# Kernel optimization log

Hardware: AMD Instinct MI355X
Metric: run time of the kernel (lower is better)

The kernel has to match this reference:

```python
import jax, jax.numpy as jnp
import numpy as np

N_NODES = 100000
N_EDGES = 1600000
IN_DIM = 256
HEAD_DIM = 64  # out_dim // num_heads = 256 // 4
NEG_SLOPE = 0.01  # F.leaky_relu default


def setup_inputs() -> dict:
    key = jax.random.key(0)
    k1, k2, k3, k4, k5, k6 = jax.random.split(key, 6)
    h = jax.random.normal(k1, (N_NODES, IN_DIM), dtype=jnp.float32)
    snorm_n = jax.random.uniform(k2, (N_NODES, 1), dtype=jnp.float32)
    fc_w = jax.random.normal(k3, (HEAD_DIM, IN_DIM), dtype=jnp.float32) * (1.0 / np.sqrt(IN_DIM))
    attn_w = jax.random.normal(k4, (1, 2 * HEAD_DIM), dtype=jnp.float32) * (1.0 / np.sqrt(2 * HEAD_DIM))
    src = jax.random.randint(k5, (N_EDGES,), 0, N_NODES, dtype=jnp.int64 if jax.config.jax_enable_x64 else jnp.int32)
    dst = jax.random.randint(k6, (N_EDGES,), 0, N_NODES, dtype=jnp.int64 if jax.config.jax_enable_x64 else jnp.int32)
    return {"h": h, "snorm_n": snorm_n, "fc_w": fc_w, "attn_w": attn_w, "src": src, "dst": dst}


def reference(h, snorm_n, fc_w, attn_w, src, dst):
    N = h.shape[0]
    z = h @ fc_w.T  # [N, d]
    d = z.shape[1]
    # attn_fc(cat([z_src, z_dst])) == z_src @ w_l + z_dst @ w_r
    w_l, w_r = attn_w[0, :d], attn_w[0, d:]
    el = z @ w_l  # [N]
    er = z @ w_r  # [N]
    e = jax.nn.leaky_relu(el[src] + er[dst], NEG_SLOPE)  # [E] edge scores
    # segment softmax over incoming edges of each dst node
    m = jax.ops.segment_max(e, dst, num_segments=N)
    m = jnp.where(jnp.isfinite(m), m, 0.0)  # empty segments -> -inf, neutralize
    ex = jnp.exp(e - m[dst])
    denom = jax.ops.segment_sum(ex, dst, num_segments=N)
    alpha = ex / denom[dst]  # [E]
    # weighted scatter-sum of source features
    h_out = jax.ops.segment_sum(alpha[:, None] * z[src], dst, num_segments=N)  # [N, d]
    h_out = h_out * snorm_n  # graph_norm
    return jax.nn.relu(h_out)
```

## Files before the change

kernel.cpp:

```cpp
#include <hip/hip_runtime.h>
#include <math.h>

#define NEG_SLOPE 0.01f
#define NB 256
#define BATCH 4096
#define HROW 264

typedef __attribute__((ext_vector_type(8))) short short8;
typedef __attribute__((ext_vector_type(4))) float f32x4;

__device__ __forceinline__ unsigned short f2bf_rne(float f) {
    unsigned u = __float_as_uint(f);
    unsigned r = 0x7fffu + ((u >> 16) & 1u);
    return (unsigned short)((u + r) >> 16);
}
__device__ __forceinline__ float bf2f(unsigned short b) {
    return __uint_as_float(((unsigned)b) << 16);
}
__device__ __forceinline__ unsigned cvtpk(float lo, float hi) {
    unsigned r;
    asm("v_cvt_pk_bf16_f32 %0, %1, %2" : "=v"(r) : "v"(lo), "v"(hi));
    return r;
}

__global__ __launch_bounds__(256) void k_hist(
    const int* __restrict__ dst, int* __restrict__ hist_blk, int n_edges,
    const float* __restrict__ fc_w,
    unsigned short* __restrict__ w_hi, unsigned short* __restrict__ w_lo, int wdim)
{
    const int tid = threadIdx.x;
    const int nbatch = (n_edges + BATCH - 1) / BATCH;
    if ((int)blockIdx.x < nbatch) {
        __shared__ int hist[NB];
        const int batch = blockIdx.x;
        hist[tid] = 0;
        __syncthreads();
        const int e0 = batch * BATCH;
        const int n = min(BATCH, n_edges - e0);
        #pragma unroll
        for (int k = 0; k < 16; ++k) {
            int j = tid + k * 256;
            if (j < n) atomicAdd(&hist[dst[e0 + j] >> 9], 1);
        }
        __syncthreads();
        hist_blk[batch * NB + tid] = hist[tid];
    } else {
        int i = (blockIdx.x - nbatch) * 256 + tid;
        if (i < wdim) {
            float f = fc_w[i];
            unsigned u = __float_as_uint(f);
            w_hi[i] = (unsigned short)(u >> 16);
            float lo = f - __uint_as_float(u & 0xffff0000u);
            w_lo[i] = f2bf_rne(lo);
        }
    }
}

__global__ __launch_bounds__(256) void k_p2loc(
    const int* __restrict__ hist_blk, int* __restrict__ bb,
    int* __restrict__ bucket_tot, int n_edges)
{
    const int tid = threadIdx.x;
    const int b = blockIdx.x;
    const int nbatch = (n_edges + BATCH - 1) / BATCH;
    __shared__ int v[512], s2[256];
    v[tid]       = (tid < nbatch)       ? hist_blk[tid * NB + b]         : 0;
    v[tid + 256] = (tid + 256 < nbatch) ? hist_blk[(tid + 256) * NB + b] : 0;
    __syncthreads();
    int pair = v[2 * tid] + v[2 * tid + 1];
    s2[tid] = pair;
    __syncthreads();
    for (int off = 1; off < 256; off <<= 1) {
        int t = (tid >= off) ? s2[tid - off] : 0;
        __syncthreads();
        s2[tid] += t;
        __syncthreads();
    }
    int e2 = s2[tid] - pair;
    if (2 * tid < nbatch)     bb[b * nbatch + 2 * tid]     = e2;
    if (2 * tid + 1 < nbatch) bb[b * nbatch + 2 * tid + 1] = e2 + v[2 * tid];
    if (tid == 255) bucket_tot[b] = s2[255];
}

__global__ __launch_bounds__(256) void k_p2a(
    const int* __restrict__ bucket_tot, int* __restrict__ bucket_base)
{
    const int tid = threadIdx.x;
    __shared__ int a[NB];
    int tot = bucket_tot[tid];
    a[tid] = tot;
    __syncthreads();
    for (int off = 1; off < NB; off <<= 1) {
        int t = (tid >= off) ? a[tid - off] : 0;
        __syncthreads();
        a[tid] += t;
        __syncthreads();
    }
    bucket_base[tid] = a[tid] - tot;
    if (tid == NB - 1) bucket_base[NB] = a[tid];
}

__global__ __launch_bounds__(256) void k_p3convgemm(
    const int* __restrict__ src, const int* __restrict__ dst,
    const int* __restrict__ bb, const int* __restrict__ bucket_base,
    unsigned* __restrict__ rec1, int n_edges,
    const float* __restrict__ h,
    const unsigned short* __restrict__ w_hi, const unsigned short* __restrict__ w_lo,
    const float* __restrict__ attn_w,
    unsigned short* __restrict__ z_bf16, float* __restrict__ el, float* __restrict__ er,
    int n_nodes)
{
    __shared__ __align__(16) char smem[24832];
    const int tid = threadIdx.x;
    const int nbatch = (n_edges + BATCH - 1) / BATCH;

    if ((int)blockIdx.x < nbatch) {
        int* hist  = (int*)smem;
        int* offs  = hist + NB;
        int* cnt2  = offs + NB;
        int* gbase = cnt2 + NB;
        unsigned* staged = (unsigned*)(gbase + NB);
        unsigned char* sbkt = (unsigned char*)(staged + BATCH);
        const int batch = blockIdx.x;
        const int e0 = batch * BATCH;
        const int n = min(BATCH, n_edges - e0);
        hist[tid] = 0; cnt2[tid] = 0;
        gbase[tid] = bucket_base[tid] + bb[tid * nbatch + batch];
        __syncthreads();
        int d[16], s[16];
        #pragma unroll
        for (int k = 0; k < 16; ++k) {
            int j = tid + k * 256;
            if (j < n) {
                d[k] = dst[e0 + j];
                s[k] = src[e0 + j];
                atomicAdd(&hist[d[k] >> 9], 1);
            } else d[k] = -1;
        }
        __syncthreads();
        int hv = hist[tid];
        for (int off = 1; off < NB; off <<= 1) {
            int t = (tid >= off) ? hist[tid - off] : 0;
            __syncthreads();
            hist[tid] += t;
            __syncthreads();
        }
        offs[tid] = hist[tid] - hv;
        __syncthreads();
        #pragma unroll
        for (int k = 0; k < 16; ++k) {
            if (d[k] >= 0) {
                int b = d[k] >> 9;
                int r = atomicAdd(&cnt2[b], 1);
                int slot = offs[b] + r;
                staged[slot] = ((unsigned)(d[k] & 511) << 17) | (unsigned)s[k];
                sbkt[slot] = (unsigned char)b;
            }
        }
        __syncthreads();
        #pragma unroll
        for (int k = 0; k < 16; ++k) {
            int j = tid + k * 256;
            if (j < n) {
                int b = sbkt[j];
                rec1[gbase[b] + (j - offs[b])] = staged[j];
            }
        }
    } else {
        unsigned short* hstage = (unsigned short*)smem;
        float* elp = (float*)(smem + 32 * HROW * 2);
        float* erp = elp + 128;
        const int tile = blockIdx.x - nbatch;
        const int lane = tid & 63;
        const int wave = tid >> 6;
        const int c    = lane & 15;
        const int g    = lane >> 4;
        const int c0   = wave * 16;

        const int n0 = tile << 5;
        float4 sv[8];
        #pragma unroll
        for (int rr = 0; rr < 8; ++rr) {
            int ridx = min(n0 + wave * 8 + rr, n_nodes - 1);
            sv[rr] = *(const float4*)(h + (size_t)ridx * 256 + lane * 4);
        }
        #pragma unroll
        for (int rr = 0; rr < 8; ++rr) {
            unsigned lo = cvtpk(sv[rr].x, sv[rr].y);
            unsigned hi = cvtpk(sv[rr].z, sv[rr].w);
            *(uint2*)&hstage[(wave * 8 + rr) * HROW + lane * 4] = make_uint2(lo, hi);
        }

        short8 bh[8], bl[8];
        #pragma unroll
        for (int t = 0; t < 8; ++t) {
            const int koff = (c0 + c) * 256 + t * 32 + g * 8;
            bh[t] = *(const short8*)(w_hi + koff);
            bl[t] = *(const short8*)(w_lo + koff);
        }
        const float wl_lane = attn_w[c0 + c];
        const float wr_lane = attn_w[64 + c0 + c];
        __syncthreads();

        f32x4 acc0 = {0.f, 0.f, 0.f, 0.f};
        f32x4 acc1 = {0.f, 0.f, 0.f, 0.f};
        #pragma unroll
        for (int t = 0; t < 8; ++t) {
            short8 a0 = *(const short8*)&hstage[c * HROW + t * 32 + g * 8];
            short8 a1 = *(const short8*)&hstage[(c + 16) * HROW + t * 32 + g * 8];
            acc0 = __builtin_amdgcn_mfma_f32_16x16x32_bf16(a0, bh[t], acc0, 0, 0, 0);
            acc1 = __builtin_amdgcn_mfma_f32_16x16x32_bf16(a1, bh[t], acc1, 0, 0, 0);
            acc0 = __builtin_amdgcn_mfma_f32_16x16x32_bf16(a0, bl[t], acc0, 0, 0, 0);
            acc1 = __builtin_amdgcn_mfma_f32_16x16x32_bf16(a1, bl[t], acc1, 0, 0, 0);
        }
        #pragma unroll
        for (int j = 0; j < 4; ++j) {
            int ra = n0 + 4 * g + j;
            int rb = ra + 16;
            if (ra < n_nodes) z_bf16[(size_t)ra * 64 + c0 + c] = f2bf_rne(acc0[j]);
            if (rb < n_nodes) z_bf16[(size_t)rb * 64 + c0 + c] = f2bf_rne(acc1[j]);
        }
        float pl0[4], pr0[4], pl1[4], pr1[4];
        #pragma unroll
        for (int j = 0; j < 4; ++j) {
            pl0[j] = acc0[j] * wl_lane; pr0[j] = acc0[j] * wr_lane;
            pl1[j] = acc1[j] * wl_lane; pr1[j] = acc1[j] * wr_lane;
        }
        #pragma unroll
        for (int off = 1; off < 16; off <<= 1) {
            #pragma unroll
            for (int j = 0; j < 4; ++j) {
                pl0[j] += __shfl_xor(pl0[j], off);
                pr0[j] += __shfl_xor(pr0[j], off);
                pl1[j] += __shfl_xor(pl1[j], off);
                pr1[j] += __shfl_xor(pr1[j], off);
            }
        }
        if (c == 0) {
            #pragma unroll
            for (int j = 0; j < 4; ++j) {
                elp[wave * 32 + 4 * g + j]      = pl0[j];
                elp[wave * 32 + 16 + 4 * g + j] = pl1[j];
                erp[wave * 32 + 4 * g + j]      = pr0[j];
                erp[wave * 32 + 16 + 4 * g + j] = pr1[j];
            }
        }
        __syncthreads();
        if (tid < 32) {
            if (n0 + tid < n_nodes)
                el[n0 + tid] = elp[tid] + elp[32 + tid] + elp[64 + tid] + elp[96 + tid];
        } else if (tid < 64) {
            int r = tid - 32;
            if (n0 + r < n_nodes)
                er[n0 + r] = erp[r] + erp[32 + r] + erp[64 + r] + erp[96 + r];
        }
    }
}

__global__ __launch_bounds__(256) void k_p4(
    const unsigned* __restrict__ rec1, const int* __restrict__ bucket_base,
    const float* __restrict__ el, const float* __restrict__ er,
    int* __restrict__ rowstart, int2* __restrict__ rec,
    int n_nodes, int n_edges)
{
    const int tid = threadIdx.x;
    const int b = blockIdx.x;
    const int beg  = bucket_base[b];
    const int endb = bucket_base[b + 1];
    const int nbuse = (n_nodes + 511) >> 9;
    __shared__ int cnt[512], offs[512], s2[256];
    cnt[tid] = 0; cnt[tid + 256] = 0;
    __syncthreads();
    for (int i = beg + tid; i < endb; i += 256)
        atomicAdd(&cnt[rec1[i] >> 17], 1);
    __syncthreads();
    int pair = cnt[2 * tid] + cnt[2 * tid + 1];
    s2[tid] = pair;
    __syncthreads();
    for (int off = 1; off < 256; off <<= 1) {
        int t = (tid >= off) ? s2[tid - off] : 0;
        __syncthreads();
        s2[tid] += t;
        __syncthreads();
    }
    int e2 = s2[tid] - pair;
    offs[2 * tid]     = e2;
    offs[2 * tid + 1] = e2 + cnt[2 * tid];
    __syncthreads();
    for (int t2 = tid; t2 < 512; t2 += 256) {
        int node = (b << 9) + t2;
        if (node < n_nodes) rowstart[node] = beg + offs[t2];
    }
    if (b == nbuse - 1 && tid == 0) rowstart[n_nodes] = n_edges;
    cnt[tid] = 0; cnt[tid + 256] = 0;
    __syncthreads();
    for (int i = beg + tid; i < endb; i += 256) {
        unsigned u = rec1[i];
        int rd = (int)(u >> 17);
        int s  = (int)(u & 0x1FFFFu);
        int r = atomicAdd(&cnt[rd], 1);
        float ev = el[s] + er[(b << 9) + rd];
        ev = (ev > 0.f) ? ev : NEG_SLOPE * ev;
        rec[beg + offs[rd] + r] = make_int2(s, __float_as_int(ev));
    }
}

__global__ __launch_bounds__(256) void k_agg(
    const int* __restrict__ rowstart, const int2* __restrict__ rec,
    const unsigned short* __restrict__ z,
    const float* __restrict__ snorm, float* __restrict__ out, int n_nodes)
{
    const int wid  = (blockIdx.x * blockDim.x + threadIdx.x) >> 6;
    const int lane = threadIdx.x & 63;
    if (wid >= n_nodes) return;
    const int t = lane & 15;
    const int g = lane >> 4;
    const int start = rowstart[wid];
    const int end   = rowstart[wid + 1];
    if (end == start) {
        if (g == 0) *(float4*)(out + (size_t)wid * 64 + t * 4) = make_float4(0.f, 0.f, 0.f, 0.f);
        return;
    }
    float denom = 0.f;
    float acc0 = 0.f, acc1 = 0.f, acc2 = 0.f, acc3 = 0.f;
    const int last = end - 1;
    for (int ib = start; ib < end; ib += 8) {
        int iA = ib + g;
        int iB = ib + 4 + g;
        bool vA = iA < end, vB = iB < end;
        int2 eA = rec[min(iA, last)];
        int2 eB = rec[min(iB, last)];
        ushort4 za = *(const ushort4*)(z + (size_t)eA.x * 64 + t * 4);
        ushort4 zb = *(const ushort4*)(z + (size_t)eB.x * 64 + t * 4);
        float wA = vA ? __expf(__int_as_float(eA.y)) : 0.f;
        float wB = vB ? __expf(__int_as_float(eB.y)) : 0.f;
        denom += wA + wB;
        acc0 = fmaf(wA, bf2f(za.x), acc0);
        acc1 = fmaf(wA, bf2f(za.y), acc1);
        acc2 = fmaf(wA, bf2f(za.z), acc2);
        acc3 = fmaf(wA, bf2f(za.w), acc3);
        acc0 = fmaf(wB, bf2f(zb.x), acc0);
        acc1 = fmaf(wB, bf2f(zb.y), acc1);
        acc2 = fmaf(wB, bf2f(zb.z), acc2);
        acc3 = fmaf(wB, bf2f(zb.w), acc3);
    }
    #pragma unroll
    for (int off = 16; off <= 32; off <<= 1) {
        denom += __shfl_xor(denom, off);
        acc0  += __shfl_xor(acc0,  off);
        acc1  += __shfl_xor(acc1,  off);
        acc2  += __shfl_xor(acc2,  off);
        acc3  += __shfl_xor(acc3,  off);
    }
    if (g == 0) {
        float s = snorm[wid] / denom;
        float4 o;
        o.x = fmaxf(acc0 * s, 0.f);
        o.y = fmaxf(acc1 * s, 0.f);
        o.z = fmaxf(acc2 * s, 0.f);
        o.w = fmaxf(acc3 * s, 0.f);
        *(float4*)(out + (size_t)wid * 64 + t * 4) = o;
    }
}

extern "C" void kernel_launch(void* const* d_in, const int* in_sizes, int n_in,
                              void* d_out, int out_size, void* d_ws, size_t ws_size,
                              hipStream_t stream)
{
    const float* h      = (const float*)d_in[0];
    const float* snorm  = (const float*)d_in[1];
    const float* fc_w   = (const float*)d_in[2];
    const float* attn_w = (const float*)d_in[3];
    const int*   src    = (const int*)d_in[4];
    const int*   dst    = (const int*)d_in[5];
    float* out = (float*)d_out;

    const int n_nodes = in_sizes[1];
    const int n_edges = in_sizes[4];
    const int wdim    = in_sizes[2];
    const int nbatch  = (n_edges + BATCH - 1) / BATCH;
    const int nprep   = (wdim + 255) / 256;
    const int ntiles  = (n_nodes + 31) >> 5;

    char* wsp = (char*)d_ws;
    size_t off = 0;
    auto alloc = [&](size_t bytes) -> void* {
        void* p = wsp + off;
        off += (bytes + 255) & ~(size_t)255;
        return p;
    };
    unsigned short* z_bf16 = (unsigned short*)alloc((size_t)n_nodes * 64 * sizeof(unsigned short));
    unsigned short* w_hi   = (unsigned short*)alloc((size_t)wdim * sizeof(unsigned short));
    unsigned short* w_lo   = (unsigned short*)alloc((size_t)wdim * sizeof(unsigned short));
    float* el        = (float*)alloc((size_t)n_nodes * sizeof(float));
    float* er        = (float*)alloc((size_t)n_nodes * sizeof(float));
    int*   hist_blk  = (int*)  alloc((size_t)nbatch * NB * sizeof(int));
    int*   bucket_tot  = (int*)alloc((size_t)NB * sizeof(int));
    int*   bucket_base = (int*)alloc((size_t)(NB + 1) * sizeof(int));
    int*   bb        = (int*)  alloc((size_t)NB * nbatch * sizeof(int));
    int*   rowstart  = (int*)  alloc(((size_t)n_nodes + 1) * sizeof(int));
    unsigned* rec1   = (unsigned*)alloc((size_t)n_edges * sizeof(unsigned));
    int2*  rec       = (int2*) alloc((size_t)n_edges * sizeof(int2));

    k_hist<<<nbatch + nprep, 256, 0, stream>>>(
        dst, hist_blk, n_edges, fc_w, w_hi, w_lo, wdim);
    k_p2loc<<<NB, 256, 0, stream>>>(hist_blk, bb, bucket_tot, n_edges);
    k_p2a<<<1, 256, 0, stream>>>(bucket_tot, bucket_base);
    k_p3convgemm<<<nbatch + ntiles, 256, 0, stream>>>(
        src, dst, bb, bucket_base, rec1, n_edges,
        h, w_hi, w_lo, attn_w, z_bf16, el, er, n_nodes);
    k_p4<<<NB, 256, 0, stream>>>(rec1, bucket_base, el, er, rowstart, rec,
                                 n_nodes, n_edges);
    k_agg<<<((size_t)n_nodes * 64 + 255) / 256, 256, 0, stream>>>(
        rowstart, rec, z_bf16, snorm, out, n_nodes);
}
```

Before: 128.1 us.

## Make GEMM blocks persistent with double-buffered prefetch of h tiles

The GEMM half of the fused partition/GEMM kernel now runs on about an eighth as many blocks. Each block loops over several 32-row tiles and loads the next tile's h rows into registers while the current tile is being computed, with two LDS buffers. This amortises the per-block loading of the bf16 weight fragments and hides global-load latency behind the MFMA work. In exchange the block uses more shared memory and there are fewer blocks to fill the GPU, which may reduce latency hiding across blocks.

```diff
diff --git a/kernel.cpp b/kernel.cpp
--- a/kernel.cpp
+++ b/kernel.cpp
@@ -110,7 +110,7 @@
     unsigned short* __restrict__ z_bf16, float* __restrict__ el, float* __restrict__ er,
     int n_nodes)
 {
-    __shared__ __align__(16) char smem[24832];
+    __shared__ __align__(16) char smem[34816];
     const int tid = threadIdx.x;
     const int nbatch = (n_edges + BATCH - 1) / BATCH;
 
@@ -167,29 +167,18 @@
             }
         }
     } else {
-        unsigned short* hstage = (unsigned short*)smem;
-        float* elp = (float*)(smem + 32 * HROW * 2);
+        unsigned short* buf0 = (unsigned short*)smem;
+        unsigned short* buf1 = buf0 + 32 * HROW;
+        float* elp = (float*)(smem + 2 * 32 * HROW * 2);
         float* erp = elp + 128;
-        const int tile = blockIdx.x - nbatch;
+        const int gblk    = blockIdx.x - nbatch;
+        const int gblocks = gridDim.x - nbatch;
         const int lane = tid & 63;
         const int wave = tid >> 6;
         const int c    = lane & 15;
         const int g    = lane >> 4;
         const int c0   = wave * 16;
-
-        const int n0 = tile << 5;
-        float4 sv[8];
-        #pragma unroll
-        for (int rr = 0; rr < 8; ++rr) {
-            int ridx = min(n0 + wave * 8 + rr, n_nodes - 1);
-            sv[rr] = *(const float4*)(h + (size_t)ridx * 256 + lane * 4);
-        }
-        #pragma unroll
-        for (int rr = 0; rr < 8; ++rr) {
-            unsigned lo = cvtpk(sv[rr].x, sv[rr].y);
-            unsigned hi = cvtpk(sv[rr].z, sv[rr].w);
-            *(uint2*)&hstage[(wave * 8 + rr) * HROW + lane * 4] = make_uint2(lo, hi);
-        }
+        const int ntiles = (n_nodes + 31) >> 5;
 
         short8 bh[8], bl[8];
         #pragma unroll
@@ -200,59 +189,90 @@
         }
         const float wl_lane = attn_w[c0 + c];
         const float wr_lane = attn_w[64 + c0 + c];
-        __syncthreads();
-
-        f32x4 acc0 = {0.f, 0.f, 0.f, 0.f};
-        f32x4 acc1 = {0.f, 0.f, 0.f, 0.f};
-        #pragma unroll
-        for (int t = 0; t < 8; ++t) {
-            short8 a0 = *(const short8*)&hstage[c * HROW + t * 32 + g * 8];
-            short8 a1 = *(const short8*)&hstage[(c + 16) * HROW + t * 32 + g * 8];
-            acc0 = __builtin_amdgcn_mfma_f32_16x16x32_bf16(a0, bh[t], acc0, 0, 0, 0);
-            acc1 = __builtin_amdgcn_mfma_f32_16x16x32_bf16(a1, bh[t], acc1, 0, 0, 0);
-            acc0 = __builtin_amdgcn_mfma_f32_16x16x32_bf16(a0, bl[t], acc0, 0, 0, 0);
-            acc1 = __builtin_amdgcn_mfma_f32_16x16x32_bf16(a1, bl[t], acc1, 0, 0, 0);
-        }
-        #pragma unroll
-        for (int j = 0; j < 4; ++j) {
-            int ra = n0 + 4 * g + j;
-            int rb = ra + 16;
-            if (ra < n_nodes) z_bf16[(size_t)ra * 64 + c0 + c] = f2bf_rne(acc0[j]);
-            if (rb < n_nodes) z_bf16[(size_t)rb * 64 + c0 + c] = f2bf_rne(acc1[j]);
-        }
-        float pl0[4], pr0[4], pl1[4], pr1[4];
-        #pragma unroll
-        for (int j = 0; j < 4; ++j) {
-            pl0[j] = acc0[j] * wl_lane; pr0[j] = acc0[j] * wr_lane;
-            pl1[j] = acc1[j] * wl_lane; pr1[j] = acc1[j] * wr_lane;
-        }
-        #pragma unroll
-        for (int off = 1; off < 16; off <<= 1) {
+
+        float4 sv[8];
+        int tile = gblk;
+        #pragma unroll
+        for (int rr = 0; rr < 8; ++rr) {
+            int ridx = min((tile << 5) + wave * 8 + rr, n_nodes - 1);
+            sv[rr] = *(const float4*)(h + (size_t)ridx * 256 + lane * 4);
+        }
+        unsigned short* bufc = buf0;
+        unsigned short* bufn = buf1;
+
+        while (true) {
+            const int n0 = tile << 5;
+            const int ntile = tile + gblocks;
+            #pragma unroll
+            for (int rr = 0; rr < 8; ++rr) {
+                unsigned lo = cvtpk(sv[rr].x, sv[rr].y);
+                unsigned hi = cvtpk(sv[rr].z, sv[rr].w);
+                *(uint2*)&bufc[(wave * 8 + rr) * HROW + lane * 4] = make_uint2(lo, hi);
+            }
+            if (ntile < ntiles) {
+                #pragma unroll
+                for (int rr = 0; rr < 8; ++rr) {
+                    int ridx = min((ntile << 5) + wave * 8 + rr, n_nodes - 1);
+                    sv[rr] = *(const float4*)(h + (size_t)ridx * 256 + lane * 4);
+                }
+            }
+            __syncthreads();
+
+            f32x4 acc0 = {0.f, 0.f, 0.f, 0.f};
+            f32x4 acc1 = {0.f, 0.f, 0.f, 0.f};
+            #pragma unroll
+            for (int t = 0; t < 8; ++t) {
+                short8 a0 = *(const short8*)&bufc[c * HROW + t * 32 + g * 8];
+                short8 a1 = *(const short8*)&bufc[(c + 16) * HROW + t * 32 + g * 8];
+                acc0 = __builtin_amdgcn_mfma_f32_16x16x32_bf16(a0, bh[t], acc0, 0, 0, 0);
+                acc1 = __builtin_amdgcn_mfma_f32_16x16x32_bf16(a1, bh[t], acc1, 0, 0, 0);
+                acc0 = __builtin_amdgcn_mfma_f32_16x16x32_bf16(a0, bl[t], acc0, 0, 0, 0);
+                acc1 = __builtin_amdgcn_mfma_f32_16x16x32_bf16(a1, bl[t], acc1, 0, 0, 0);
+            }
             #pragma unroll
             for (int j = 0; j < 4; ++j) {
-                pl0[j] += __shfl_xor(pl0[j], off);
-                pr0[j] += __shfl_xor(pr0[j], off);
-                pl1[j] += __shfl_xor(pl1[j], off);
-                pr1[j] += __shfl_xor(pr1[j], off);
-            }
-        }
-        if (c == 0) {
+                int ra = n0 + 4 * g + j;
+                int rb = ra + 16;
+                if (ra < n_nodes) z_bf16[(size_t)ra * 64 + c0 + c] = f2bf_rne(acc0[j]);
+                if (rb < n_nodes) z_bf16[(size_t)rb * 64 + c0 + c] = f2bf_rne(acc1[j]);
+            }
+            float pl0[4], pr0[4], pl1[4], pr1[4];
             #pragma unroll
             for (int j = 0; j < 4; ++j) {
-                elp[wave * 32 + 4 * g + j]      = pl0[j];
-                elp[wave * 32 + 16 + 4 * g + j] = pl1[j];
-                erp[wave * 32 + 4 * g + j]      = pr0[j];
-                erp[wave * 32 + 16 + 4 * g + j] = pr1[j];
-            }
-        }
-        __syncthreads();
-        if (tid < 32) {
-            if (n0 + tid < n_nodes)
-                el[n0 + tid] = elp[tid] + elp[32 + tid] + elp[64 + tid] + elp[96 + tid];
-        } else if (tid < 64) {
-            int r = tid - 32;
-            if (n0 + r < n_nodes)
-                er[n0 + r] = erp[r] + erp[32 + r] + erp[64 + r] + erp[96 + r];
+                pl0[j] = acc0[j] * wl_lane; pr0[j] = acc0[j] * wr_lane;
+                pl1[j] = acc1[j] * wl_lane; pr1[j] = acc1[j] * wr_lane;
+            }
+            #pragma unroll
+            for (int off = 1; off < 16; off <<= 1) {
+                #pragma unroll
+                for (int j = 0; j < 4; ++j) {
+                    pl0[j] += __shfl_xor(pl0[j], off);
+                    pr0[j] += __shfl_xor(pr0[j], off);
+                    pl1[j] += __shfl_xor(pl1[j], off);
+                    pr1[j] += __shfl_xor(pr1[j], off);
+                }
+            }
+            if (c == 0) {
+                #pragma unroll
+                for (int j = 0; j < 4; ++j) {
+                    elp[wave * 32 + 4 * g + j]      = pl0[j];
+                    elp[wave * 32 + 16 + 4 * g + j] = pl1[j];
+                    erp[wave * 32 + 4 * g + j]      = pr0[j];
+                    erp[wave * 32 + 16 + 4 * g + j] = pr1[j];
+                }
+            }
+            __syncthreads();
+            if (tid < 32) {
+                if (n0 + tid < n_nodes)
+                    el[n0 + tid] = elp[tid] + elp[32 + tid] + elp[64 + tid] + elp[96 + tid];
+            } else if (tid < 64) {
+                int r = tid - 32;
+                if (n0 + r < n_nodes)
+                    er[n0 + r] = erp[r] + erp[32 + r] + erp[64 + r] + erp[96 + r];
+            }
+            if (ntile >= ntiles) break;
+            tile = ntile;
+            unsigned short* tmp = bufc; bufc = bufn; bufn = tmp;
         }
     }
 }
@@ -381,6 +401,7 @@
     const int nbatch  = (n_edges + BATCH - 1) / BATCH;
     const int nprep   = (wdim + 255) / 256;
     const int ntiles  = (n_nodes + 31) >> 5;
+    const int gblocks = (ntiles + 7) / 8;
 
     char* wsp = (char*)d_ws;
     size_t off = 0;
@@ -406,7 +427,7 @@
         dst, hist_blk, n_edges, fc_w, w_hi, w_lo, wdim);
     k_p2loc<<<NB, 256, 0, stream>>>(hist_blk, bb, bucket_tot, n_edges);
     k_p2a<<<1, 256, 0, stream>>>(bucket_tot, bucket_base);
-    k_p3convgemm<<<nbatch + ntiles, 256, 0, stream>>>(
+    k_p3convgemm<<<nbatch + gblocks, 256, 0, stream>>>(
         src, dst, bb, bucket_base, rec1, n_edges,
         h, w_hi, w_lo, attn_w, z_bf16, el, er, n_nodes);
     k_p4<<<NB, 256, 0, stream>>>(rec1, bucket_base, el, er, rowstart, rec,
```

Measured after the change: 130.0 us. About the same (+1.4%).

## Make node GEMM persistent with double-buffered async global-to-LDS prefetch

Applied to the files above, without the earlier changes.

Replaces one-tile-per-block GEMM with a fixed grid of 512 persistent blocks that loop over 32-row tiles. h rows are loaded directly into LDS with global_load_lds into two 32 KB buffers with a swizzle, and the next tiles are prefetched while the current one is computed. fp32 to bf16 conversion moves to after the LDS read. LDS use rises to about 65 KB per block, which also reduces occupancy for the edge-bucketing blocks sharing this kernel.

```diff
diff --git a/kernel.cpp b/kernel.cpp
--- a/kernel.cpp
+++ b/kernel.cpp
@@ -4,7 +4,7 @@
 #define NEG_SLOPE 0.01f
 #define NB 256
 #define BATCH 4096
-#define HROW 264
+#define GEMM_BLOCKS 512
 
 typedef __attribute__((ext_vector_type(8))) short short8;
 typedef __attribute__((ext_vector_type(4))) float f32x4;
@@ -21,6 +21,14 @@
     unsigned r;
     asm("v_cvt_pk_bf16_f32 %0, %1, %2" : "=v"(r) : "v"(lo), "v"(hi));
     return r;
+}
+__device__ __forceinline__ short8 pack8(float4 a, float4 b) {
+    union { unsigned u[4]; short8 s; } r;
+    r.u[0] = cvtpk(a.x, a.y);
+    r.u[1] = cvtpk(a.z, a.w);
+    r.u[2] = cvtpk(b.x, b.y);
+    r.u[3] = cvtpk(b.z, b.w);
+    return r.s;
 }
 
 __global__ __launch_bounds__(256) void k_hist(
@@ -110,7 +118,7 @@
     unsigned short* __restrict__ z_bf16, float* __restrict__ el, float* __restrict__ er,
     int n_nodes)
 {
-    __shared__ __align__(16) char smem[24832];
+    __shared__ __align__(16) char smem[66560];
     const int tid = threadIdx.x;
     const int nbatch = (n_edges + BATCH - 1) / BATCH;
 
@@ -167,29 +175,17 @@
             }
         }
     } else {
-        unsigned short* hstage = (unsigned short*)smem;
-        float* elp = (float*)(smem + 32 * HROW * 2);
+        float* elp = (float*)(smem + 65536);
         float* erp = elp + 128;
-        const int tile = blockIdx.x - nbatch;
+        const int gblk    = blockIdx.x - nbatch;
+        const int gblocks = gridDim.x - nbatch;
         const int lane = tid & 63;
         const int wave = tid >> 6;
         const int c    = lane & 15;
         const int g    = lane >> 4;
+        const int cx   = c & 7;
         const int c0   = wave * 16;
-
-        const int n0 = tile << 5;
-        float4 sv[8];
-        #pragma unroll
-        for (int rr = 0; rr < 8; ++rr) {
-            int ridx = min(n0 + wave * 8 + rr, n_nodes - 1);
-            sv[rr] = *(const float4*)(h + (size_t)ridx * 256 + lane * 4);
-        }
-        #pragma unroll
-        for (int rr = 0; rr < 8; ++rr) {
-            unsigned lo = cvtpk(sv[rr].x, sv[rr].y);
-            unsigned hi = cvtpk(sv[rr].z, sv[rr].w);
-            *(uint2*)&hstage[(wave * 8 + rr) * HROW + lane * 4] = make_uint2(lo, hi);
-        }
+        const int ntiles = (n_nodes + 31) >> 5;
 
         short8 bh[8], bl[8];
         #pragma unroll
@@ -200,59 +196,100 @@
         }
         const float wl_lane = attn_w[c0 + c];
         const float wr_lane = attn_w[64 + c0 + c];
-        __syncthreads();
-
-        f32x4 acc0 = {0.f, 0.f, 0.f, 0.f};
-        f32x4 acc1 = {0.f, 0.f, 0.f, 0.f};
-        #pragma unroll
-        for (int t = 0; t < 8; ++t) {
-            short8 a0 = *(const short8*)&hstage[c * HROW + t * 32 + g * 8];
-            short8 a1 = *(const short8*)&hstage[(c + 16) * HROW + t * 32 + g * 8];
-            acc0 = __builtin_amdgcn_mfma_f32_16x16x32_bf16(a0, bh[t], acc0, 0, 0, 0);
-            acc1 = __builtin_amdgcn_mfma_f32_16x16x32_bf16(a1, bh[t], acc1, 0, 0, 0);
-            acc0 = __builtin_amdgcn_mfma_f32_16x16x32_bf16(a0, bl[t], acc0, 0, 0, 0);
-            acc1 = __builtin_amdgcn_mfma_f32_16x16x32_bf16(a1, bl[t], acc1, 0, 0, 0);
-        }
-        #pragma unroll
-        for (int j = 0; j < 4; ++j) {
-            int ra = n0 + 4 * g + j;
-            int rb = ra + 16;
-            if (ra < n_nodes) z_bf16[(size_t)ra * 64 + c0 + c] = f2bf_rne(acc0[j]);
-            if (rb < n_nodes) z_bf16[(size_t)rb * 64 + c0 + c] = f2bf_rne(acc1[j]);
-        }
-        float pl0[4], pr0[4], pl1[4], pr1[4];
-        #pragma unroll
-        for (int j = 0; j < 4; ++j) {
-            pl0[j] = acc0[j] * wl_lane; pr0[j] = acc0[j] * wr_lane;
-            pl1[j] = acc1[j] * wl_lane; pr1[j] = acc1[j] * wr_lane;
-        }
-        #pragma unroll
-        for (int off = 1; off < 16; off <<= 1) {
+
+        auto stage = [&](int tt, char* slot) {
+            #pragma unroll
+            for (int rr = 0; rr < 8; ++rr) {
+                int r = wave * 8 + rr;
+                int grow = tt * 32 + r;
+                if (grow > n_nodes - 1) grow = n_nodes - 1;
+                const float* gp = h + (size_t)grow * 256 + ((lane ^ (r & 7)) << 2);
+                __builtin_amdgcn_global_load_lds(
+                    (const __attribute__((address_space(1))) void*)gp,
+                    (__attribute__((address_space(3))) void*)(slot + r * 1024),
+                    16, 0, 0);
+            }
+        };
+
+        const int nt = (ntiles - 1 - gblk) / gblocks + 1;
+        stage(gblk, smem);
+        stage(gblk + gblocks, smem + 32768);
+
+        for (int k = 0; k < nt; ++k) {
+            const int tt = gblk + k * gblocks;
+            const int n0 = tt << 5;
+            if (k == 0) { asm volatile("s_waitcnt vmcnt(8)" ::: "memory"); }
+            else        { asm volatile("s_waitcnt vmcnt(16)" ::: "memory"); }
+            __builtin_amdgcn_sched_barrier(0);
+            __builtin_amdgcn_s_barrier();
+            __builtin_amdgcn_sched_barrier(0);
+
+            const char* base = smem + (k & 1) * 32768;
+            const char* r0b = base + c * 1024;
+            const char* r1b = base + (c + 16) * 1024;
+            f32x4 acc0 = {0.f, 0.f, 0.f, 0.f};
+            f32x4 acc1 = {0.f, 0.f, 0.f, 0.f};
+            #pragma unroll
+            for (int t = 0; t < 8; ++t) {
+                const int j0 = t * 8 + g * 2;
+                float4 x0 = *(const float4*)(r0b + ((j0    ) ^ cx) * 16);
+                float4 x1 = *(const float4*)(r0b + ((j0 + 1) ^ cx) * 16);
+                float4 y0 = *(const float4*)(r1b + ((j0    ) ^ cx) * 16);
+                float4 y1 = *(const float4*)(r1b + ((j0 + 1) ^ cx) * 16);
+                short8 a0 = pack8(x0, x1);
+                short8 a1 = pack8(y0, y1);
+                acc0 = __builtin_amdgcn_mfma_f32_16x16x32_bf16(a0, bh[t], acc0, 0, 0, 0);
+                acc1 = __builtin_amdgcn_mfma_f32_16x16x32_bf16(a1, bh[t], acc1, 0, 0, 0);
+                acc0 = __builtin_amdgcn_mfma_f32_16x16x32_bf16(a0, bl[t], acc0, 0, 0, 0);
+                acc1 = __builtin_amdgcn_mfma_f32_16x16x32_bf16(a1, bl[t], acc1, 0, 0, 0);
+            }
             #pragma unroll
             for (int j = 0; j < 4; ++j) {
-                pl0[j] += __shfl_xor(pl0[j], off);
-                pr0[j] += __shfl_xor(pr0[j], off);
-                pl1[j] += __shfl_xor(pl1[j], off);
-                pr1[j] += __shfl_xor(pr1[j], off);
-            }
-        }
-        if (c == 0) {
+                int ra = n0 + 4 * g + j;
+                int rb = ra + 16;
+                if (ra < n_nodes) z_bf16[(size_t)ra * 64 + c0 + c] = f2bf_rne(acc0[j]);
+                if (rb < n_nodes) z_bf16[(size_t)rb * 64 + c0 + c] = f2bf_rne(acc1[j]);
+            }
+            float pl0[4], pr0[4], pl1[4], pr1[4];
             #pragma unroll
             for (int j = 0; j < 4; ++j) {
-                elp[wave * 32 + 4 * g + j]      = pl0[j];
-                elp[wave * 32 + 16 + 4 * g + j] = pl1[j];
-                erp[wave * 32 + 4 * g + j]      = pr0[j];
-                erp[wave * 32 + 16 + 4 * g + j] = pr1[j];
-            }
-        }
-        __syncthreads();
-        if (tid < 32) {
-            if (n0 + tid < n_nodes)
-                el[n0 + tid] = elp[tid] + elp[32 + tid] + elp[64 + tid] + elp[96 + tid];
-        } else if (tid < 64) {
-            int r = tid - 32;
-            if (n0 + r < n_nodes)
-                er[n0 + r] = erp[r] + erp[32 + r] + erp[64 + r] + erp[96 + r];
+                pl0[j] = acc0[j] * wl_lane; pr0[j] = acc0[j] * wr_lane;
+                pl1[j] = acc1[j] * wl_lane; pr1[j] = acc1[j] * wr_lane;
+            }
+            #pragma unroll
+            for (int off = 1; off < 16; off <<= 1) {
+                #pragma unroll
+                for (int j = 0; j < 4; ++j) {
+                    pl0[j] += __shfl_xor(pl0[j], off);
+                    pr0[j] += __shfl_xor(pr0[j], off);
+                    pl1[j] += __shfl_xor(pl1[j], off);
+                    pr1[j] += __shfl_xor(pr1[j], off);
+                }
+            }
+            if (c == 0) {
+                #pragma unroll
+                for (int j = 0; j < 4; ++j) {
+                    elp[wave * 32 + 4 * g + j]      = pl0[j];
+                    elp[wave * 32 + 16 + 4 * g + j] = pl1[j];
+                    erp[wave * 32 + 4 * g + j]      = pr0[j];
+                    erp[wave * 32 + 16 + 4 * g + j] = pr1[j];
+                }
+            }
+            asm volatile("s_waitcnt lgkmcnt(0)" ::: "memory");
+            __builtin_amdgcn_sched_barrier(0);
+            __builtin_amdgcn_s_barrier();
+            __builtin_amdgcn_sched_barrier(0);
+
+            stage(gblk + (k + 2) * gblocks, (char*)smem + (k & 1) * 32768);
+
+            if (tid < 32) {
+                if (n0 + tid < n_nodes)
+                    el[n0 + tid] = elp[tid] + elp[32 + tid] + elp[64 + tid] + elp[96 + tid];
+            } else if (tid < 64) {
+                int r = tid - 32;
+                if (n0 + r < n_nodes)
+                    er[n0 + r] = erp[r] + erp[32 + r] + erp[64 + r] + erp[96 + r];
+            }
         }
     }
 }
@@ -380,7 +417,6 @@
     const int wdim    = in_sizes[2];
     const int nbatch  = (n_edges + BATCH - 1) / BATCH;
     const int nprep   = (wdim + 255) / 256;
-    const int ntiles  = (n_nodes + 31) >> 5;
 
     char* wsp = (char*)d_ws;
     size_t off = 0;
@@ -406,7 +442,7 @@
         dst, hist_blk, n_edges, fc_w, w_hi, w_lo, wdim);
     k_p2loc<<<NB, 256, 0, stream>>>(hist_blk, bb, bucket_tot, n_edges);
     k_p2a<<<1, 256, 0, stream>>>(bucket_tot, bucket_base);
-    k_p3convgemm<<<nbatch + ntiles, 256, 0, stream>>>(
+    k_p3convgemm<<<nbatch + GEMM_BLOCKS, 256, 0, stream>>>(
         src, dst, bb, bucket_base, rec1, n_edges,
         h, w_hi, w_lo, attn_w, z_bf16, el, er, n_nodes);
     k_p4<<<NB, 256, 0, stream>>>(rec1, bucket_base, el, er, rowstart, rec,
```

After: 133.2 us. +4.0%, slower.

## Fuse bucket-base scan into p2loc via last-block ticket; unroll aggregation loop

Applied to the files above, without the earlier changes.

Removes the separate single-block k_p2a launch. The last k_p2loc block to finish, chosen by an atomic ticket counter that k_hist resets, now performs the bucket-total exclusive scan. This removes one kernel launch and its dependency gap, in exchange for threadfences and an atomic per block. Separately, the aggregation loop gains an unguarded 16-edge fast path that issues four gathers per lane group before falling back to the masked 8-edge tail loop, which exposes more memory-level parallelism.

```diff
diff --git a/kernel.cpp b/kernel.cpp
--- a/kernel.cpp
+++ b/kernel.cpp
@@ -26,10 +26,12 @@
 __global__ __launch_bounds__(256) void k_hist(
     const int* __restrict__ dst, int* __restrict__ hist_blk, int n_edges,
     const float* __restrict__ fc_w,
-    unsigned short* __restrict__ w_hi, unsigned short* __restrict__ w_lo, int wdim)
+    unsigned short* __restrict__ w_hi, unsigned short* __restrict__ w_lo, int wdim,
+    int* __restrict__ p2ctr)
 {
     const int tid = threadIdx.x;
     const int nbatch = (n_edges + BATCH - 1) / BATCH;
+    if (blockIdx.x == 0 && tid == 0) *p2ctr = 0;
     if ((int)blockIdx.x < nbatch) {
         __shared__ int hist[NB];
         const int batch = blockIdx.x;
@@ -58,12 +60,14 @@
 
 __global__ __launch_bounds__(256) void k_p2loc(
     const int* __restrict__ hist_blk, int* __restrict__ bb,
-    int* __restrict__ bucket_tot, int n_edges)
+    int* __restrict__ bucket_tot, int* __restrict__ bucket_base,
+    int* __restrict__ p2ctr, int n_edges)
 {
     const int tid = threadIdx.x;
     const int b = blockIdx.x;
     const int nbatch = (n_edges + BATCH - 1) / BATCH;
     __shared__ int v[512], s2[256];
+    __shared__ int ticket;
     v[tid]       = (tid < nbatch)       ? hist_blk[tid * NB + b]         : 0;
     v[tid + 256] = (tid + 256 < nbatch) ? hist_blk[(tid + 256) * NB + b] : 0;
     __syncthreads();
@@ -80,24 +84,24 @@
     if (2 * tid < nbatch)     bb[b * nbatch + 2 * tid]     = e2;
     if (2 * tid + 1 < nbatch) bb[b * nbatch + 2 * tid + 1] = e2 + v[2 * tid];
     if (tid == 255) bucket_tot[b] = s2[255];
-}
-
-__global__ __launch_bounds__(256) void k_p2a(
-    const int* __restrict__ bucket_tot, int* __restrict__ bucket_base)
-{
-    const int tid = threadIdx.x;
-    __shared__ int a[NB];
-    int tot = bucket_tot[tid];
-    a[tid] = tot;
-    __syncthreads();
-    for (int off = 1; off < NB; off <<= 1) {
-        int t = (tid >= off) ? a[tid - off] : 0;
-        __syncthreads();
-        a[tid] += t;
-        __syncthreads();
-    }
-    bucket_base[tid] = a[tid] - tot;
-    if (tid == NB - 1) bucket_base[NB] = a[tid];
+    __threadfence();
+    __syncthreads();
+    if (tid == 0) ticket = atomicAdd(p2ctr, 1);
+    __syncthreads();
+    if (ticket == NB - 1) {
+        __threadfence();
+        int tot = bucket_tot[tid];
+        s2[tid] = tot;
+        __syncthreads();
+        for (int off = 1; off < NB; off <<= 1) {
+            int t = (tid >= off) ? s2[tid - off] : 0;
+            __syncthreads();
+            s2[tid] += t;
+            __syncthreads();
+        }
+        bucket_base[tid] = s2[tid] - tot;
+        if (tid == NB - 1) bucket_base[NB] = s2[tid];
+    }
 }
 
 __global__ __launch_bounds__(256) void k_p3convgemm(
@@ -324,7 +328,31 @@
     float denom = 0.f;
     float acc0 = 0.f, acc1 = 0.f, acc2 = 0.f, acc3 = 0.f;
     const int last = end - 1;
-    for (int ib = start; ib < end; ib += 8) {
+    int ib = start;
+    for (; ib + 16 <= end; ib += 16) {
+        int2 e0 = rec[ib + g];
+        int2 e1 = rec[ib + 4 + g];
+        int2 e2 = rec[ib + 8 + g];
+        int2 e3 = rec[ib + 12 + g];
+        ushort4 z0 = *(const ushort4*)(z + (size_t)e0.x * 64 + t * 4);
+        ushort4 z1 = *(const ushort4*)(z + (size_t)e1.x * 64 + t * 4);
+        ushort4 z2 = *(const ushort4*)(z + (size_t)e2.x * 64 + t * 4);
+        ushort4 z3 = *(const ushort4*)(z + (size_t)e3.x * 64 + t * 4);
+        float w0 = __expf(__int_as_float(e0.y));
+        float w1 = __expf(__int_as_float(e1.y));
+        float w2 = __expf(__int_as_float(e2.y));
+        float w3 = __expf(__int_as_float(e3.y));
+        denom += (w0 + w1) + (w2 + w3);
+        acc0 = fmaf(w0, bf2f(z0.x), acc0); acc1 = fmaf(w0, bf2f(z0.y), acc1);
+        acc2 = fmaf(w0, bf2f(z0.z), acc2); acc3 = fmaf(w0, bf2f(z0.w), acc3);
+        acc0 = fmaf(w1, bf2f(z1.x), acc0); acc1 = fmaf(w1, bf2f(z1.y), acc1);
+        acc2 = fmaf(w1, bf2f(z1.z), acc2); acc3 = fmaf(w1, bf2f(z1.w), acc3);
+        acc0 = fmaf(w2, bf2f(z2.x), acc0); acc1 = fmaf(w2, bf2f(z2.y), acc1);
+        acc2 = fmaf(w2, bf2f(z2.z), acc2); acc3 = fmaf(w2, bf2f(z2.w), acc3);
+        acc0 = fmaf(w3, bf2f(z3.x), acc0); acc1 = fmaf(w3, bf2f(z3.y), acc1);
+        acc2 = fmaf(w3, bf2f(z3.z), acc2); acc3 = fmaf(w3, bf2f(z3.w), acc3);
+    }
+    for (; ib < end; ib += 8) {
         int iA = ib + g;
         int iB = ib + 4 + g;
         bool vA = iA < end, vB = iB < end;
@@ -397,15 +425,16 @@
     int*   hist_blk  = (int*)  alloc((size_t)nbatch * NB * sizeof(int));
     int*   bucket_tot  = (int*)alloc((size_t)NB * sizeof(int));
     int*   bucket_base = (int*)alloc((size_t)(NB + 1) * sizeof(int));
+    int*   p2ctr     = (int*)  alloc(256);
     int*   bb        = (int*)  alloc((size_t)NB * nbatch * sizeof(int));
     int*   rowstart  = (int*)  alloc(((size_t)n_nodes + 1) * sizeof(int));
     unsigned* rec1   = (unsigned*)alloc((size_t)n_edges * sizeof(unsigned));
     int2*  rec       = (int2*) alloc((size_t)n_edges * sizeof(int2));
 
     k_hist<<<nbatch + nprep, 256, 0, stream>>>(
-        dst, hist_blk, n_edges, fc_w, w_hi, w_lo, wdim);
-    k_p2loc<<<NB, 256, 0, stream>>>(hist_blk, bb, bucket_tot, n_edges);
-    k_p2a<<<1, 256, 0, stream>>>(bucket_tot, bucket_base);
+        dst, hist_blk, n_edges, fc_w, w_hi, w_lo, wdim, p2ctr);
+    k_p2loc<<<NB, 256, 0, stream>>>(hist_blk, bb, bucket_tot, bucket_base,
+                                    p2ctr, n_edges);
     k_p3convgemm<<<nbatch + ntiles, 256, 0, stream>>>(
         src, dst, bb, bucket_base, rec1, n_edges,
         h, w_hi, w_lo, attn_w, z_bf16, el, er, n_nodes);
```

New measurement: 143.8 us. 1.12x slower.
